# Kernel optimization log

Hardware: AMD Instinct MI355X
Metric: run time of the kernel (lower is better)

## Reference

```python
import jax, jax.numpy as jnp
import numpy as np
import math

N, E = 50000, 1600000
IN, HID, OUT, ED, H = 128, 32, 64, 64, 4
HC = H * HID  # 128, input dim of second layer


def setup_inputs() -> dict:
    key = jax.random.key(0)
    ks = jax.random.split(key, 32)
    w = lambda k, shape: (jax.random.normal(k, shape, jnp.float32) * 0.05)
    inp = {
        "x": w(ks[0], (N, IN)),
        "edge_feats": w(ks[1], (E, ED)),
        "edge_index": jax.random.randint(ks[2], (2, E), 0, N, jnp.int32),
        # layer 1: TransformerConv(IN -> HID, heads=H, concat=True, edge_dim=ED)
        "Wq1": w(ks[3], (IN, HC)), "bq1": w(ks[4], (HC,)),
        "Wk1": w(ks[5], (IN, HC)), "bk1": w(ks[6], (HC,)),
        "Wv1": w(ks[7], (IN, HC)), "bv1": w(ks[8], (HC,)),
        "We1": w(ks[9], (ED, HC)),  # lin_edge has no bias in PyG
        "Ws1": w(ks[10], (IN, HC)), "bs1": w(ks[11], (HC,)),
        # layer 2: TransformerConv(HC -> OUT, heads=1, concat=False, edge_dim=ED)
        "Wq2": w(ks[12], (HC, OUT)), "bq2": w(ks[13], (OUT,)),
        "Wk2": w(ks[14], (HC, OUT)), "bk2": w(ks[15], (OUT,)),
        "Wv2": w(ks[16], (HC, OUT)), "bv2": w(ks[17], (OUT,)),
        "We2": w(ks[18], (ED, OUT)),
        "Ws2": w(ks[19], (HC, OUT)), "bs2": w(ks[20], (OUT,)),
    }
    return inp


def tconv(x, src, dst, ef, Wq, bq, Wk, bk, Wv, bv, We, Ws, bs, heads, ch, concat):
    """PyG TransformerConv (beta=False, root_weight=True), eval mode."""
    n = x.shape[0]
    q = (x @ Wq + bq).reshape(n, heads, ch)
    k = (x @ Wk + bk).reshape(n, heads, ch)
    v = (x @ Wv + bv).reshape(n, heads, ch)
    e = (ef @ We).reshape(-1, heads, ch)           # [E,H,C]
    k_j = k[src] + e                                # gather + edge bias
    v_j = v[src] + e
    alpha = jnp.einsum("ehc,ehc->eh", q[dst], k_j) / math.sqrt(ch)  # [E,H]
    # segment softmax over destination nodes
    m = jax.lax.stop_gradient(jax.ops.segment_max(alpha, dst, num_segments=n))
    a = jnp.exp(alpha - m[dst])
    den = jax.ops.segment_sum(a, dst, num_segments=n)
    a = a / den[dst]
    msg = v_j * a[..., None]                        # [E,H,C]
    out = jax.ops.segment_sum(msg, dst, num_segments=n)  # [N,H,C]
    out = out.reshape(n, heads * ch) if concat else out.mean(axis=1)
    return out + x @ Ws + bs                        # root/skip connection


def reference(x, edge_feats, edge_index, Wq1, bq1, Wk1, bk1, Wv1, bv1, We1, Ws1, bs1,
              Wq2, bq2, Wk2, bk2, Wv2, bv2, We2, Ws2, bs2):
    src, dst = edge_index[0], edge_index[1]
    h = tconv(x, src, dst, edge_feats, Wq1, bq1, Wk1, bk1, Wv1, bv1, We1, Ws1, bs1,
              H, HID, True)
    h = jax.nn.relu(h)  # dropout=0.0 (eval) -> identity
    out = tconv(h, src, dst, edge_feats, Wq2, bq2, Wk2, bk2, Wv2, bv2, We2, Ws2, bs2,
                1, OUT, False)
    return out
```

## Files before the change

### kernel.cpp

```cpp
#include <hip/hip_runtime.h>

#define NN 50000
#define EE 1600000

__device__ inline float b2f(unsigned short u) {
    return __uint_as_float(((unsigned)u) << 16);
}
__device__ inline unsigned short f2bf(float f) {
    unsigned u = __float_as_uint(f);
    unsigned r = 0x7fffu + ((u >> 16) & 1u);
    return (unsigned short)((u + r) >> 16);
}
__device__ inline void stv(float* p, size_t i, float v) { p[i] = v; }
__device__ inline void stv(unsigned short* p, size_t i, float v) { p[i] = f2bf(v); }

__global__ void sniff_kernel(const void* w, int* flags) {
    int lane = threadIdx.x;
    const unsigned short* u = (const unsigned short*)w;
    int bad = 0;
    for (int i = lane; i < 256; i += 64) {
        float f = b2f(u[i]);
        if (!(fabsf(f) < 2.0f)) bad++;
    }
    unsigned long long m = __ballot(bad > 0);
    if (lane == 0) {
        flags[0] = (__popcll(m) > 8) ? 1 : 0;
        flags[1] = 0;
    }
}

struct WTab {
    const void* p[18];
    int off[18];
    int sz[18];
};
__global__ void __launch_bounds__(256) convert_kernel(WTab t, const int* __restrict__ flags,
                                                      unsigned short* __restrict__ dst) {
    int f32 = flags[0];
    int ti = blockIdx.y;
    int i = blockIdx.x * 256 + threadIdx.x;
    if (i < t.sz[ti]) {
        dst[t.off[ti] + i] = f32 ? f2bf(((const float*)t.p[ti])[i])
                                 : ((const unsigned short*)t.p[ti])[i];
    }
}

__global__ void __launch_bounds__(256) count_kernel(const int* __restrict__ dst,
                                                    int* __restrict__ cnt) {
    int e = blockIdx.x * 256 + threadIdx.x;
    if (e < EE) atomicAdd(&cnt[dst[e]], 1);
}

__global__ void __launch_bounds__(1024) scan_kernel(int* __restrict__ cntfill,
                                                    int* __restrict__ rowptr) {
    __shared__ int s[1024];
    __shared__ int carry_s;
    int tid = threadIdx.x;
    if (tid == 0) carry_s = 0;
    __syncthreads();
    for (int base = 0; base < NN; base += 4096) {
        int i0 = base + tid * 4;
        int v0 = (i0 + 0 < NN) ? cntfill[i0 + 0] : 0;
        int v1 = (i0 + 1 < NN) ? cntfill[i0 + 1] : 0;
        int v2 = (i0 + 2 < NN) ? cntfill[i0 + 2] : 0;
        int v3 = (i0 + 3 < NN) ? cntfill[i0 + 3] : 0;
        int tsum = v0 + v1 + v2 + v3;
        s[tid] = tsum;
        __syncthreads();
        for (int off = 1; off < 1024; off <<= 1) {
            int t = (tid >= off) ? s[tid - off] : 0;
            __syncthreads();
            s[tid] += t;
            __syncthreads();
        }
        int carry = carry_s;
        int excl = carry + s[tid] - tsum;
        int e0 = excl, e1 = excl + v0, e2 = e1 + v1, e3 = e2 + v2;
        if (i0 + 0 < NN) { rowptr[i0 + 0] = e0; cntfill[i0 + 0] = e0; }
        if (i0 + 1 < NN) { rowptr[i0 + 1] = e1; cntfill[i0 + 1] = e1; }
        if (i0 + 2 < NN) { rowptr[i0 + 2] = e2; cntfill[i0 + 2] = e2; }
        if (i0 + 3 < NN) { rowptr[i0 + 3] = e3; cntfill[i0 + 3] = e3; }
        __syncthreads();
        if (tid == 1023) carry_s = carry + s[1023];
        __syncthreads();
    }
    if (tid == 0) rowptr[NN] = carry_s;
}

__global__ void __launch_bounds__(256) fill_kernel(const int* __restrict__ dst,
                                                   int* __restrict__ cntfill,
                                                   int* __restrict__ perm) {
    int e = blockIdx.x * 256 + threadIdx.x;
    if (e < EE) {
        int p = atomicAdd(&cntfill[dst[e]], 1);
        perm[p] = e;
    }
}

template <typename TO, int K, int OD, int TR>
__global__ void __launch_bounds__(256) gemm_node(const void* __restrict__ X,
                                                 const int* __restrict__ flagp,
                                                 const unsigned short* __restrict__ W,
                                                 const unsigned short* __restrict__ bias,
                                                 TO* __restrict__ C, int nrows,
                                                 int ldc, int cstride, int coff) {
    constexpr int TRP = TR + 4;
    __shared__ unsigned short Ws[K * OD];
    __shared__ float Xs[K * TRP];
    int tid = threadIdx.x;
    int xf32 = *flagp;
    for (int i = tid; i < K * OD; i += 256) Ws[i] = W[i];
    int row0 = blockIdx.x * TR;
    const float* Xf = (const float*)X;
    const unsigned short* Xu = (const unsigned short*)X;
    for (int i = tid; i < TR * K; i += 256) {
        int r = i / K, kk = i % K;
        int rr = row0 + r;
        float vv = 0.f;
        if (rr < nrows) {
            size_t idx = (size_t)rr * K + kk;
            vv = xf32 ? Xf[idx] : b2f(Xu[idx]);
        }
        Xs[kk * TRP + r] = vv;
    }
    __syncthreads();
    constexpr int CG = OD / 4;
    int rg = tid / CG, cg = tid % CG;
    int r0 = rg * 4, c0 = cg * 4;
    float acc[4][4] = {};
#pragma unroll 4
    for (int kk = 0; kk < K; ++kk) {
        const float4 xv = *(const float4*)&Xs[kk * TRP + r0];
        ushort4 wu = *(const ushort4*)&Ws[kk * OD + c0];
        float xa[4] = {xv.x, xv.y, xv.z, xv.w};
        float wb[4] = {b2f(wu.x), b2f(wu.y), b2f(wu.z), b2f(wu.w)};
#pragma unroll
        for (int i2 = 0; i2 < 4; i2++)
#pragma unroll
            for (int j2 = 0; j2 < 4; j2++) acc[i2][j2] += xa[i2] * wb[j2];
    }
    float bb[4];
#pragma unroll
    for (int j2 = 0; j2 < 4; j2++) bb[j2] = b2f(bias[c0 + j2]);
#pragma unroll
    for (int i2 = 0; i2 < 4; i2++) {
        int rr = row0 + r0 + i2;
        if (rr < nrows) {
#pragma unroll
            for (int j2 = 0; j2 < 4; j2++)
                stv(C, (size_t)rr * ldc + (size_t)(c0 + j2) * cstride + coff,
                    acc[i2][j2] + bb[j2]);
        }
    }
}

__global__ void __launch_bounds__(256) qe1_kernel(const unsigned short* __restrict__ q,
                                                  const unsigned short* __restrict__ We,
                                                  float* __restrict__ qe) {
    __shared__ float Ws[64 * 129];
    __shared__ float qs[8 * 128];
    int tid = threadIdx.x;
    for (int i = tid; i < 64 * 128; i += 256) Ws[(i / 128) * 129 + (i % 128)] = b2f(We[i]);
    int n0 = blockIdx.x * 8;
    for (int i = tid; i < 8 * 128; i += 256) {
        int n = n0 + (i >> 7);
        qs[i] = (n < NN) ? b2f(q[(size_t)n * 128 + (i & 127)]) : 0.f;
    }
    __syncthreads();
    int h = tid >> 6, d = tid & 63;
    for (int nl = 0; nl < 8; ++nl) {
        int n = n0 + nl;
        if (n < NN) {
            float acc = 0.f;
#pragma unroll
            for (int c = 0; c < 32; ++c)
                acc += qs[nl * 128 + h * 32 + c] * Ws[d * 129 + h * 32 + c];
            qe[(size_t)n * 256 + h * 64 + d] = acc;
        }
    }
}

__global__ void __launch_bounds__(256) qe2_kernel(const unsigned short* __restrict__ q,
                                                  const unsigned short* __restrict__ We,
                                                  float* __restrict__ qe) {
    __shared__ float Ws[64 * 65];
    __shared__ float qs[4 * 64];
    int tid = threadIdx.x;
    for (int i = tid; i < 64 * 64; i += 256) Ws[(i / 64) * 65 + (i % 64)] = b2f(We[i]);
    int n0 = blockIdx.x * 4;
    {
        int n = n0 + (tid >> 6);
        qs[tid] = (n < NN) ? b2f(q[(size_t)n * 64 + (tid & 63)]) : 0.f;
    }
    __syncthreads();
    int nl = tid >> 6, d = tid & 63;
    int n = n0 + nl;
    if (n < NN) {
        float acc = 0.f;
#pragma unroll
        for (int c = 0; c < 64; ++c) acc += qs[nl * 64 + c] * Ws[d * 65 + c];
        qe[(size_t)n * 64 + d] = acc;
    }
}

__global__ void __launch_bounds__(256) node_pass1(
    const int* __restrict__ rowptr, const int* __restrict__ perm,
    const int* __restrict__ src, const unsigned short* __restrict__ q,
    const unsigned short* __restrict__ kv,
    const float* __restrict__ qe, const void* __restrict__ efp,
    const int* __restrict__ flagp, float* __restrict__ av, float* __restrict__ wef) {
    int lane = threadIdx.x & 63;
    int node = (blockIdx.x * 256 + threadIdx.x) >> 6;
    if (node >= NN) return;
    int ef32 = *flagp;
    const float* efF = (const float*)efp;
    const unsigned short* efU = (const unsigned short*)efp;
    int h = lane & 3;
    int dq = lane >> 2;
    int c1 = h * 32 + dq, c2 = c1 + 16;
    float qa = b2f(q[(size_t)node * 128 + c1]);
    float qb = b2f(q[(size_t)node * 128 + c2]);
    float4 qm = *(const float4*)(qe + (size_t)node * 256 + h * 64 + 4 * dq);
    float m = -__builtin_inff(), l = 0.f, a1 = 0.f, a2 = 0.f;
    float w0 = 0.f, w1 = 0.f, w2 = 0.f, w3 = 0.f;
    int beg = rowptr[node], end = rowptr[node + 1];
    const float rs = 0.17677669529663687f;

    int nn4 = (end - beg) & ~3;
    int lim = beg + nn4;
    int i = beg;
    int ee[4], ss[4];
    if (nn4 > 0) {
#pragma unroll
        for (int u = 0; u < 4; ++u) ee[u] = perm[i + u];
#pragma unroll
        for (int u = 0; u < 4; ++u) ss[u] = src[ee[u]];
    }
    for (; i < lim; i += 4) {
        unsigned kua[4], kub[4];
        float f0[4], f1[4], f2[4], f3[4];
#pragma unroll
        for (int u = 0; u < 4; ++u) {
            const unsigned short* kr = kv + (size_t)ss[u] * 256;
            kua[u] = *(const unsigned*)(kr + 2 * c1);
            kub[u] = *(const unsigned*)(kr + 2 * c2);
        }
        if (ef32) {
#pragma unroll
            for (int u = 0; u < 4; ++u) {
                float4 fv = *(const float4*)(efF + (size_t)ee[u] * 64 + 4 * dq);
                f0[u] = fv.x; f1[u] = fv.y; f2[u] = fv.z; f3[u] = fv.w;
            }
        } else {
#pragma unroll
            for (int u = 0; u < 4; ++u) {
                ushort4 fu = *(const ushort4*)(efU + (size_t)ee[u] * 64 + 4 * dq);
                f0[u] = b2f(fu.x); f1[u] = b2f(fu.y); f2[u] = b2f(fu.z); f3[u] = b2f(fu.w);
            }
        }
        if (i + 8 <= lim) {
#pragma unroll
            for (int u = 0; u < 4; ++u) ee[u] = perm[i + 4 + u];
#pragma unroll
            for (int u = 0; u < 4; ++u) ss[u] = src[ee[u]];
        }
        float t[4];
#pragma unroll
        for (int u = 0; u < 4; ++u) {
            float ka = b2f((unsigned short)(kua[u] & 0xffffu));
            float kb = b2f((unsigned short)(kub[u] & 0xffffu));
            float tt = qa * ka + qb * kb + qm.x * f0[u] + qm.y * f1[u] +
                       qm.z * f2[u] + qm.w * f3[u];
            tt += __shfl_xor(tt, 4);
            tt += __shfl_xor(tt, 8);
            tt += __shfl_xor(tt, 16);
            tt += __shfl_xor(tt, 32);
            t[u] = tt * rs;
        }
        float mn = fmaxf(fmaxf(fmaxf(t[0], t[1]), fmaxf(t[2], t[3])), m);
        float sc = __expf(m - mn);
        float w[4];
#pragma unroll
        for (int u = 0; u < 4; ++u) w[u] = __expf(t[u] - mn);
        m = mn;
        l = l * sc + ((w[0] + w[1]) + (w[2] + w[3]));
        float sa1 = 0.f, sa2 = 0.f, sw0 = 0.f, sw1 = 0.f, sw2 = 0.f, sw3 = 0.f;
#pragma unroll
        for (int u = 0; u < 4; ++u) {
            float va = b2f((unsigned short)(kua[u] >> 16));
            float vb = b2f((unsigned short)(kub[u] >> 16));
            sa1 += w[u] * va; sa2 += w[u] * vb;
            sw0 += w[u] * f0[u]; sw1 += w[u] * f1[u];
            sw2 += w[u] * f2[u]; sw3 += w[u] * f3[u];
        }
        a1 = a1 * sc + sa1; a2 = a2 * sc + sa2;
        w0 = w0 * sc + sw0; w1 = w1 * sc + sw1;
        w2 = w2 * sc + sw2; w3 = w3 * sc + sw3;
    }
    for (; i < end; ++i) {
        int e = perm[i];
        int sj = src[e];
        const unsigned short* kr = kv + (size_t)sj * 256;
        unsigned kua = *(const unsigned*)(kr + 2 * c1);
        unsigned kub = *(const unsigned*)(kr + 2 * c2);
        float f0s, f1s, f2s, f3s;
        if (ef32) {
            float4 fv = *(const float4*)(efF + (size_t)e * 64 + 4 * dq);
            f0s = fv.x; f1s = fv.y; f2s = fv.z; f3s = fv.w;
        } else {
            ushort4 fu = *(const ushort4*)(efU + (size_t)e * 64 + 4 * dq);
            f0s = b2f(fu.x); f1s = b2f(fu.y); f2s = b2f(fu.z); f3s = b2f(fu.w);
        }
        float ka = b2f((unsigned short)(kua & 0xffffu));
        float kb = b2f((unsigned short)(kub & 0xffffu));
        float tt = qa * ka + qb * kb + qm.x * f0s + qm.y * f1s + qm.z * f2s + qm.w * f3s;
        tt += __shfl_xor(tt, 4);
        tt += __shfl_xor(tt, 8);
        tt += __shfl_xor(tt, 16);
        tt += __shfl_xor(tt, 32);
        float alpha = tt * rs;
        float mn = fmaxf(m, alpha);
        float sc = __expf(m - mn);
        float w = __expf(alpha - mn);
        m = mn;
        l = l * sc + w;
        float va = b2f((unsigned short)(kua >> 16));
        float vb = b2f((unsigned short)(kub >> 16));
        a1 = a1 * sc + w * va;
        a2 = a2 * sc + w * vb;
        w0 = w0 * sc + w * f0s; w1 = w1 * sc + w * f1s;
        w2 = w2 * sc + w * f2s; w3 = w3 * sc + w * f3s;
    }
    float inv = (l > 0.f) ? 1.f / l : 0.f;
    av[(size_t)node * 128 + c1] = a1 * inv;
    av[(size_t)node * 128 + c2] = a2 * inv;
    float4 wout = make_float4(w0 * inv, w1 * inv, w2 * inv, w3 * inv);
    *(float4*)(wef + (size_t)node * 256 + h * 64 + 4 * dq) = wout;
}

__global__ void __launch_bounds__(256) node_pass2(
    const int* __restrict__ rowptr, const int* __restrict__ perm,
    const int* __restrict__ src, const unsigned short* __restrict__ q,
    const unsigned short* __restrict__ kv,
    const float* __restrict__ qe, const void* __restrict__ efp,
    const int* __restrict__ flagp, float* __restrict__ av, float* __restrict__ wef) {
    int lane = threadIdx.x & 63;
    int node = (blockIdx.x * 256 + threadIdx.x) >> 6;
    if (node >= NN) return;
    int ef32 = *flagp;
    const float* efF = (const float*)efp;
    const unsigned short* efU = (const unsigned short*)efp;
    float qa = b2f(q[(size_t)node * 64 + lane]);
    float qj = qe[(size_t)node * 64 + lane];
    float m = -__builtin_inff(), l = 0.f, a1 = 0.f, w0 = 0.f;
    int beg = rowptr[node], end = rowptr[node + 1];

    int nn4 = (end - beg) & ~3;
    int lim = beg + nn4;
    int i = beg;
    int ee[4], ss[4];
    if (nn4 > 0) {
#pragma unroll
        for (int u = 0; u < 4; ++u) ee[u] = perm[i + u];
#pragma unroll
        for (int u = 0; u < 4; ++u) ss[u] = src[ee[u]];
    }
    for (; i < lim; i += 4) {
        unsigned ku[4];
        float fj[4];
#pragma unroll
        for (int u = 0; u < 4; ++u)
            ku[u] = *(const unsigned*)(kv + (size_t)ss[u] * 128 + 2 * lane);
        if (ef32) {
#pragma unroll
            for (int u = 0; u < 4; ++u) fj[u] = efF[(size_t)ee[u] * 64 + lane];
        } else {
#pragma unroll
            for (int u = 0; u < 4; ++u) fj[u] = b2f(efU[(size_t)ee[u] * 64 + lane]);
        }
        if (i + 8 <= lim) {
#pragma unroll
            for (int u = 0; u < 4; ++u) ee[u] = perm[i + 4 + u];
#pragma unroll
            for (int u = 0; u < 4; ++u) ss[u] = src[ee[u]];
        }
        float t[4];
#pragma unroll
        for (int u = 0; u < 4; ++u) {
            float kk = b2f((unsigned short)(ku[u] & 0xffffu));
            float tt = qa * kk + qj * fj[u];
            tt += __shfl_xor(tt, 1);
            tt += __shfl_xor(tt, 2);
            tt += __shfl_xor(tt, 4);
            tt += __shfl_xor(tt, 8);
            tt += __shfl_xor(tt, 16);
            tt += __shfl_xor(tt, 32);
            t[u] = tt * 0.125f;
        }
        float mn = fmaxf(fmaxf(fmaxf(t[0], t[1]), fmaxf(t[2], t[3])), m);
        float sc = __expf(m - mn);
        float w[4];
#pragma unroll
        for (int u = 0; u < 4; ++u) w[u] = __expf(t[u] - mn);
        m = mn;
        l = l * sc + ((w[0] + w[1]) + (w[2] + w[3]));
        float sa = 0.f, sw = 0.f;
#pragma unroll
        for (int u = 0; u < 4; ++u) {
            float vv = b2f((unsigned short)(ku[u] >> 16));
            sa += w[u] * vv;
            sw += w[u] * fj[u];
        }
        a1 = a1 * sc + sa;
        w0 = w0 * sc + sw;
    }
    for (; i < end; ++i) {
        int e = perm[i];
        int sj = src[e];
        unsigned ku = *(const unsigned*)(kv + (size_t)sj * 128 + 2 * lane);
        float fj = ef32 ? efF[(size_t)e * 64 + lane] : b2f(efU[(size_t)e * 64 + lane]);
        float kk = b2f((unsigned short)(ku & 0xffffu));
        float tt = qa * kk + qj * fj;
        tt += __shfl_xor(tt, 1);
        tt += __shfl_xor(tt, 2);
        tt += __shfl_xor(tt, 4);
        tt += __shfl_xor(tt, 8);
        tt += __shfl_xor(tt, 16);
        tt += __shfl_xor(tt, 32);
        float alpha = tt * 0.125f;
        float mn = fmaxf(m, alpha);
        float sc = __expf(m - mn);
        float w = __expf(alpha - mn);
        m = mn;
        l = l * sc + w;
        float vv = b2f((unsigned short)(ku >> 16));
        a1 = a1 * sc + w * vv;
        w0 = w0 * sc + w * fj;
    }
    float inv = (l > 0.f) ? 1.f / l : 0.f;
    av[(size_t)node * 64 + lane] = a1 * inv;
    wef[(size_t)node * 64 + lane] = w0 * inv;
}

__global__ void __launch_bounds__(256) ep1_kernel(const float* __restrict__ av,
                                                  const float* __restrict__ wef,
                                                  const float* __restrict__ s1,
                                                  const unsigned short* __restrict__ We,
                                                  unsigned short* __restrict__ hout) {
    __shared__ float Ws[64 * 128];
    int tid = threadIdx.x;
    for (int i = tid; i < 64 * 128; i += 256) Ws[i] = b2f(We[i]);
    __syncthreads();
    int nl = tid >> 7;
    int c = tid & 127;
    int g = c >> 5;
    for (int it = 0; it < 8; ++it) {
        int n = blockIdx.x * 16 + it * 2 + nl;
        if (n < NN) {
            const float* wr = wef + (size_t)n * 256 + g * 64;
            float acc = 0.f;
#pragma unroll
            for (int d = 0; d < 64; ++d) acc += wr[d] * Ws[d * 128 + c];
            float val = av[(size_t)n * 128 + c] + acc + s1[(size_t)n * 128 + c];
            hout[(size_t)n * 128 + c] = f2bf(fmaxf(val, 0.f));
        }
    }
}

__global__ void __launch_bounds__(256) ep2_kernel(const float* __restrict__ av,
                                                  const float* __restrict__ wef,
                                                  const float* __restrict__ s2,
                                                  const unsigned short* __restrict__ We,
                                                  float* __restrict__ out) {
    __shared__ float Ws[64 * 64];
    int tid = threadIdx.x;
    for (int i = tid; i < 64 * 64; i += 256) Ws[i] = b2f(We[i]);
    __syncthreads();
    int nl = tid >> 6;
    int c = tid & 63;
    for (int it = 0; it < 4; ++it) {
        int n = blockIdx.x * 16 + it * 4 + nl;
        if (n < NN) {
            const float* wr = wef + (size_t)n * 64;
            float acc = 0.f;
#pragma unroll
            for (int d = 0; d < 64; ++d) acc += wr[d] * Ws[d * 64 + c];
            float val = av[(size_t)n * 64 + c] + acc + s2[(size_t)n * 64 + c];
            out[(size_t)n * 64 + c] = val;
        }
    }
}

extern "C" void kernel_launch(void* const* d_in, const int* in_sizes, int n_in,
                              void* d_out, int out_size, void* d_ws, size_t ws_size,
                              hipStream_t stream) {
    (void)in_sizes; (void)n_in; (void)out_size; (void)ws_size;
    const int* eidx = (const int*)d_in[2];
    const int* src = eidx;
    const int* dst = eidx + EE;

    char* p = (char*)d_ws;
    auto alloc = [&](size_t bytes) {
        void* r = (void*)p;
        p += (bytes + 255) & ~(size_t)255;
        return r;
    };
    unsigned short* wts = (unsigned short*)alloc(111360 * 2);
    int* flags          = (int*)alloc(256);
    int* rowptr         = (int*)alloc((size_t)(NN + 1) * 4);
    int* cntfill        = (int*)alloc((size_t)(NN + 1) * 4);
    int* perm           = (int*)alloc((size_t)EE * 4);
    unsigned short* q1  = (unsigned short*)alloc((size_t)NN * 128 * 2);
    unsigned short* kv1 = (unsigned short*)alloc((size_t)NN * 256 * 2);
    float* qe           = (float*)alloc((size_t)NN * 256 * 4);
    float* av           = (float*)alloc((size_t)NN * 128 * 4);
    float* wef          = (float*)alloc((size_t)NN * 256 * 4);

    WTab tab;
    int off = 0;
    const int wsz[18] = {16384, 128, 16384, 128, 16384, 128, 8192, 16384, 128,
                         8192, 64, 8192, 64, 8192, 64, 4096, 8192, 64};
    int offs[18];
    for (int i = 0; i < 18; ++i) {
        tab.p[i] = d_in[3 + i];
        tab.sz[i] = wsz[i];
        tab.off[i] = off;
        offs[i] = off;
        off += wsz[i];
    }
    const unsigned short* Wq1c = wts + offs[0];
    const unsigned short* bq1c = wts + offs[1];
    const unsigned short* Wk1c = wts + offs[2];
    const unsigned short* bk1c = wts + offs[3];
    const unsigned short* Wv1c = wts + offs[4];
    const unsigned short* bv1c = wts + offs[5];
    const unsigned short* We1c = wts + offs[6];
    const unsigned short* Ws1c = wts + offs[7];
    const unsigned short* bs1c = wts + offs[8];
    const unsigned short* Wq2c = wts + offs[9];
    const unsigned short* bq2c = wts + offs[10];
    const unsigned short* Wk2c = wts + offs[11];
    const unsigned short* bk2c = wts + offs[12];
    const unsigned short* Wv2c = wts + offs[13];
    const unsigned short* bv2c = wts + offs[14];
    const unsigned short* We2c = wts + offs[15];
    const unsigned short* Ws2c = wts + offs[16];
    const unsigned short* bs2c = wts + offs[17];

    hipMemsetAsync(cntfill, 0, (size_t)(NN + 1) * 4, stream);
    sniff_kernel<<<1, 64, 0, stream>>>(d_in[3], flags);
    convert_kernel<<<dim3(64, 18), 256, 0, stream>>>(tab, flags, wts);
    count_kernel<<<EE / 256, 256, 0, stream>>>(dst, cntfill);
    scan_kernel<<<1, 1024, 0, stream>>>(cntfill, rowptr);
    fill_kernel<<<EE / 256, 256, 0, stream>>>(dst, cntfill, perm);

    int g1 = (NN + 31) / 32;
    gemm_node<unsigned short, 128, 128, 32><<<g1, 256, 0, stream>>>(d_in[0], flags, Wq1c, bq1c, q1, NN, 128, 1, 0);
    gemm_node<unsigned short, 128, 128, 32><<<g1, 256, 0, stream>>>(d_in[0], flags, Wk1c, bk1c, kv1, NN, 256, 2, 0);
    gemm_node<unsigned short, 128, 128, 32><<<g1, 256, 0, stream>>>(d_in[0], flags, Wv1c, bv1c, kv1, NN, 256, 2, 1);
    qe1_kernel<<<(NN + 7) / 8, 256, 0, stream>>>(q1, We1c, qe);
    node_pass1<<<(NN + 3) / 4, 256, 0, stream>>>(rowptr, perm, src, q1, kv1, qe,
                                                 d_in[1], flags, av, wef);
    float* s1 = qe;
    gemm_node<float, 128, 128, 32><<<g1, 256, 0, stream>>>(d_in[0], flags, Ws1c, bs1c, s1, NN, 128, 1, 0);
    unsigned short* h = kv1;
    ep1_kernel<<<(NN + 15) / 16, 256, 0, stream>>>(av, wef, s1, We1c, h);

    unsigned short* q2 = q1;
    unsigned short* kv2 = kv1 + (size_t)NN * 128;
    float* s2 = qe;
    float* qe2 = av;
    float* av2 = av + (size_t)NN * 64;
    float* wef2 = wef;
    int g2 = (NN + 63) / 64;
    gemm_node<unsigned short, 128, 64, 64><<<g2, 256, 0, stream>>>(h, flags + 1, Wq2c, bq2c, q2, NN, 64, 1, 0);
    gemm_node<unsigned short, 128, 64, 64><<<g2, 256, 0, stream>>>(h, flags + 1, Wk2c, bk2c, kv2, NN, 128, 2, 0);
    gemm_node<unsigned short, 128, 64, 64><<<g2, 256, 0, stream>>>(h, flags + 1, Wv2c, bv2c, kv2, NN, 128, 2, 1);
    gemm_node<float, 128, 64, 64><<<g2, 256, 0, stream>>>(h, flags + 1, Ws2c, bs2c, s2, NN, 64, 1, 0);
    qe2_kernel<<<(NN + 3) / 4, 256, 0, stream>>>(q2, We2c, qe2);
    node_pass2<<<(NN + 3) / 4, 256, 0, stream>>>(rowptr, perm, src, q2, kv2, qe2,
                                                 d_in[1], flags, av2, wef2);
    ep2_kernel<<<(NN + 15) / 16, 256, 0, stream>>>(av2, wef2, s2, We2c,
                                                   (float*)d_out);
}
```

Before: 1.676 ms.

## Pre-permute edge features and sources into CSR order, double-buffer neighbor loads

Adds an edge_gather kernel that writes src indices and bf16 edge features in destination-sorted order once. Both node passes then read these contiguously instead of going through perm and gathering fp32 edge rows twice. Layer-1 K/V are stored in an interleaved layout so one 8-byte load fetches both k and v values per lane. The node loops are restructured into an A/B double-buffered prefetch pipeline. The trade-off is an extra 200MB-class permute write/read pass and bf16 rounding of edge features when they arrive as fp32.

```diff
diff --git a/kernel.cpp b/kernel.cpp
--- a/kernel.cpp
+++ b/kernel.cpp
@@ -97,7 +97,36 @@
     }
 }
 
-template <typename TO, int K, int OD, int TR>
+__global__ void __launch_bounds__(256) edge_gather(const int* __restrict__ perm,
+                                                   const int* __restrict__ src,
+                                                   const void* __restrict__ efp,
+                                                   const int* __restrict__ flagp,
+                                                   int* __restrict__ src_perm,
+                                                   unsigned short* __restrict__ efperm) {
+    int ef32 = *flagp;
+    int tid = threadIdx.x;
+    int j = tid & 15;
+    int local = tid >> 4;
+    const float* efF = (const float*)efp;
+    const unsigned short* efU = (const unsigned short*)efp;
+    for (int pass = 0; pass < 4; ++pass) {
+        int i = blockIdx.x * 64 + pass * 16 + local;
+        if (i < EE) {
+            int e = perm[i];
+            if (j == 0) src_perm[i] = src[e];
+            ushort4 o;
+            if (ef32) {
+                float4 f = *(const float4*)(efF + (size_t)e * 64 + j * 4);
+                o.x = f2bf(f.x); o.y = f2bf(f.y); o.z = f2bf(f.z); o.w = f2bf(f.w);
+            } else {
+                o = *(const ushort4*)(efU + (size_t)e * 64 + j * 4);
+            }
+            *(ushort4*)(efperm + (size_t)i * 64 + j * 4) = o;
+        }
+    }
+}
+
+template <typename TO, int K, int OD, int TR, int LAYOUT = 0>
 __global__ void __launch_bounds__(256) gemm_node(const void* __restrict__ X,
                                                  const int* __restrict__ flagp,
                                                  const unsigned short* __restrict__ W,
@@ -147,9 +176,19 @@
         int rr = row0 + r0 + i2;
         if (rr < nrows) {
 #pragma unroll
-            for (int j2 = 0; j2 < 4; j2++)
-                stv(C, (size_t)rr * ldc + (size_t)(c0 + j2) * cstride + coff,
-                    acc[i2][j2] + bb[j2]);
+            for (int j2 = 0; j2 < 4; j2++) {
+                size_t idx;
+                if constexpr (LAYOUT == 0) {
+                    idx = (size_t)rr * ldc + (size_t)(c0 + j2) * cstride + coff;
+                } else {
+                    int c = c0 + j2;
+                    int hh = c >> 5, r = c & 31;
+                    idx = (size_t)rr * 256 +
+                          (size_t)((hh * 16 + (r & 15)) * 4 + (r >> 4) +
+                                   (LAYOUT == 2 ? 2 : 0));
+                }
+                stv(C, idx, acc[i2][j2] + bb[j2]);
+            }
         }
     }
 }
@@ -203,21 +242,59 @@
     }
 }
 
+__device__ __forceinline__ void np1_step(const uint2 (&kvd)[4], const ushort4 (&efd)[4],
+                                         float qa, float qb, const float4& qm, float rs,
+                                         float& m, float& l, float& a1, float& a2,
+                                         float& w0, float& w1, float& w2, float& w3) {
+    float t[4];
+    float f0[4], f1[4], f2[4], f3[4];
+#pragma unroll
+    for (int u = 0; u < 4; ++u) {
+        float ka = b2f((unsigned short)(kvd[u].x & 0xffffu));
+        float kb = b2f((unsigned short)(kvd[u].x >> 16));
+        f0[u] = b2f(efd[u].x); f1[u] = b2f(efd[u].y);
+        f2[u] = b2f(efd[u].z); f3[u] = b2f(efd[u].w);
+        float tt = qa * ka + qb * kb + qm.x * f0[u] + qm.y * f1[u] +
+                   qm.z * f2[u] + qm.w * f3[u];
+        tt += __shfl_xor(tt, 4);
+        tt += __shfl_xor(tt, 8);
+        tt += __shfl_xor(tt, 16);
+        tt += __shfl_xor(tt, 32);
+        t[u] = tt * rs;
+    }
+    float mn = fmaxf(fmaxf(fmaxf(t[0], t[1]), fmaxf(t[2], t[3])), m);
+    float sc = __expf(m - mn);
+    float w[4];
+#pragma unroll
+    for (int u = 0; u < 4; ++u) w[u] = __expf(t[u] - mn);
+    m = mn;
+    l = l * sc + ((w[0] + w[1]) + (w[2] + w[3]));
+    float sa1 = 0.f, sa2 = 0.f, sw0 = 0.f, sw1 = 0.f, sw2 = 0.f, sw3 = 0.f;
+#pragma unroll
+    for (int u = 0; u < 4; ++u) {
+        float va = b2f((unsigned short)(kvd[u].y & 0xffffu));
+        float vb = b2f((unsigned short)(kvd[u].y >> 16));
+        sa1 += w[u] * va; sa2 += w[u] * vb;
+        sw0 += w[u] * f0[u]; sw1 += w[u] * f1[u];
+        sw2 += w[u] * f2[u]; sw3 += w[u] * f3[u];
+    }
+    a1 = a1 * sc + sa1; a2 = a2 * sc + sa2;
+    w0 = w0 * sc + sw0; w1 = w1 * sc + sw1;
+    w2 = w2 * sc + sw2; w3 = w3 * sc + sw3;
+}
+
 __global__ void __launch_bounds__(256) node_pass1(
-    const int* __restrict__ rowptr, const int* __restrict__ perm,
-    const int* __restrict__ src, const unsigned short* __restrict__ q,
-    const unsigned short* __restrict__ kv,
-    const float* __restrict__ qe, const void* __restrict__ efp,
-    const int* __restrict__ flagp, float* __restrict__ av, float* __restrict__ wef) {
+    const int* __restrict__ rowptr, const int* __restrict__ srcp,
+    const unsigned short* __restrict__ q, const unsigned short* __restrict__ kv,
+    const float* __restrict__ qe, const unsigned short* __restrict__ efperm,
+    float* __restrict__ av, float* __restrict__ wef) {
     int lane = threadIdx.x & 63;
     int node = (blockIdx.x * 256 + threadIdx.x) >> 6;
     if (node >= NN) return;
-    int ef32 = *flagp;
-    const float* efF = (const float*)efp;
-    const unsigned short* efU = (const unsigned short*)efp;
     int h = lane & 3;
     int dq = lane >> 2;
     int c1 = h * 32 + dq, c2 = c1 + 16;
+    int kvoff = (h * 16 + dq) * 4;
     float qa = b2f(q[(size_t)node * 128 + c1]);
     float qb = b2f(q[(size_t)node * 128 + c2]);
     float4 qm = *(const float4*)(qe + (size_t)node * 256 + h * 64 + 4 * dq);
@@ -225,94 +302,72 @@
     float w0 = 0.f, w1 = 0.f, w2 = 0.f, w3 = 0.f;
     int beg = rowptr[node], end = rowptr[node + 1];
     const float rs = 0.17677669529663687f;
-
-    int nn4 = (end - beg) & ~3;
-    int lim = beg + nn4;
-    int i = beg;
-    int ee[4], ss[4];
-    if (nn4 > 0) {
-#pragma unroll
-        for (int u = 0; u < 4; ++u) ee[u] = perm[i + u];
-#pragma unroll
-        for (int u = 0; u < 4; ++u) ss[u] = src[ee[u]];
-    }
-    for (; i < lim; i += 4) {
-        unsigned kua[4], kub[4];
-        float f0[4], f1[4], f2[4], f3[4];
-#pragma unroll
-        for (int u = 0; u < 4; ++u) {
-            const unsigned short* kr = kv + (size_t)ss[u] * 256;
-            kua[u] = *(const unsigned*)(kr + 2 * c1);
-            kub[u] = *(const unsigned*)(kr + 2 * c2);
-        }
-        if (ef32) {
-#pragma unroll
-            for (int u = 0; u < 4; ++u) {
-                float4 fv = *(const float4*)(efF + (size_t)ee[u] * 64 + 4 * dq);
-                f0[u] = fv.x; f1[u] = fv.y; f2[u] = fv.z; f3[u] = fv.w;
+    int ng = (end - beg) >> 2;
+
+    int ssA[4], ssB[4];
+    uint2 kvA[4], kvB[4];
+    ushort4 efA[4], efB[4];
+
+    if (ng > 0) {
+#pragma unroll
+        for (int u = 0; u < 4; ++u) ssA[u] = srcp[beg + u];
+#pragma unroll
+        for (int u = 0; u < 4; ++u)
+            kvA[u] = *(const uint2*)(kv + (size_t)ssA[u] * 256 + kvoff);
+#pragma unroll
+        for (int u = 0; u < 4; ++u)
+            efA[u] = *(const ushort4*)(efperm + (size_t)(beg + u) * 64 + 4 * dq);
+        if (ng > 1) {
+#pragma unroll
+            for (int u = 0; u < 4; ++u) ssB[u] = srcp[beg + 4 + u];
+        }
+        int g = 0;
+        while (true) {
+            bool nextB = (g + 1 < ng);
+            if (nextB) {
+                int ib = beg + ((g + 1) << 2);
+#pragma unroll
+                for (int u = 0; u < 4; ++u)
+                    kvB[u] = *(const uint2*)(kv + (size_t)ssB[u] * 256 + kvoff);
+#pragma unroll
+                for (int u = 0; u < 4; ++u)
+                    efB[u] = *(const ushort4*)(efperm + (size_t)(ib + u) * 64 + 4 * dq);
+                if (g + 2 < ng) {
+                    int ib2 = beg + ((g + 2) << 2);
+#pragma unroll
+                    for (int u = 0; u < 4; ++u) ssA[u] = srcp[ib2 + u];
+                }
             }
-        } else {
-#pragma unroll
-            for (int u = 0; u < 4; ++u) {
-                ushort4 fu = *(const ushort4*)(efU + (size_t)ee[u] * 64 + 4 * dq);
-                f0[u] = b2f(fu.x); f1[u] = b2f(fu.y); f2[u] = b2f(fu.z); f3[u] = b2f(fu.w);
+            np1_step(kvA, efA, qa, qb, qm, rs, m, l, a1, a2, w0, w1, w2, w3);
+            if (!nextB) { ++g; break; }
+            ++g;
+            bool nextA = (g + 1 < ng);
+            if (nextA) {
+                int ib = beg + ((g + 1) << 2);
+#pragma unroll
+                for (int u = 0; u < 4; ++u)
+                    kvA[u] = *(const uint2*)(kv + (size_t)ssA[u] * 256 + kvoff);
+#pragma unroll
+                for (int u = 0; u < 4; ++u)
+                    efA[u] = *(const ushort4*)(efperm + (size_t)(ib + u) * 64 + 4 * dq);
+                if (g + 2 < ng) {
+                    int ib2 = beg + ((g + 2) << 2);
+#pragma unroll
+                    for (int u = 0; u < 4; ++u) ssB[u] = srcp[ib2 + u];
+                }
             }
-        }
-        if (i + 8 <= lim) {
-#pragma unroll
-            for (int u = 0; u < 4; ++u) ee[u] = perm[i + 4 + u];
-#pragma unroll
-            for (int u = 0; u < 4; ++u) ss[u] = src[ee[u]];
-        }
-        float t[4];
-#pragma unroll
-        for (int u = 0; u < 4; ++u) {
-            float ka = b2f((unsigned short)(kua[u] & 0xffffu));
-            float kb = b2f((unsigned short)(kub[u] & 0xffffu));
-            float tt = qa * ka + qb * kb + qm.x * f0[u] + qm.y * f1[u] +
-                       qm.z * f2[u] + qm.w * f3[u];
-            tt += __shfl_xor(tt, 4);
-            tt += __shfl_xor(tt, 8);
-            tt += __shfl_xor(tt, 16);
-            tt += __shfl_xor(tt, 32);
-            t[u] = tt * rs;
-        }
-        float mn = fmaxf(fmaxf(fmaxf(t[0], t[1]), fmaxf(t[2], t[3])), m);
-        float sc = __expf(m - mn);
-        float w[4];
-#pragma unroll
-        for (int u = 0; u < 4; ++u) w[u] = __expf(t[u] - mn);
-        m = mn;
-        l = l * sc + ((w[0] + w[1]) + (w[2] + w[3]));
-        float sa1 = 0.f, sa2 = 0.f, sw0 = 0.f, sw1 = 0.f, sw2 = 0.f, sw3 = 0.f;
-#pragma unroll
-        for (int u = 0; u < 4; ++u) {
-            float va = b2f((unsigned short)(kua[u] >> 16));
-            float vb = b2f((unsigned short)(kub[u] >> 16));
-            sa1 += w[u] * va; sa2 += w[u] * vb;
-            sw0 += w[u] * f0[u]; sw1 += w[u] * f1[u];
-            sw2 += w[u] * f2[u]; sw3 += w[u] * f3[u];
-        }
-        a1 = a1 * sc + sa1; a2 = a2 * sc + sa2;
-        w0 = w0 * sc + sw0; w1 = w1 * sc + sw1;
-        w2 = w2 * sc + sw2; w3 = w3 * sc + sw3;
-    }
-    for (; i < end; ++i) {
-        int e = perm[i];
-        int sj = src[e];
-        const unsigned short* kr = kv + (size_t)sj * 256;
-        unsigned kua = *(const unsigned*)(kr + 2 * c1);
-        unsigned kub = *(const unsigned*)(kr + 2 * c2);
-        float f0s, f1s, f2s, f3s;
-        if (ef32) {
-            float4 fv = *(const float4*)(efF + (size_t)e * 64 + 4 * dq);
-            f0s = fv.x; f1s = fv.y; f2s = fv.z; f3s = fv.w;
-        } else {
-            ushort4 fu = *(const ushort4*)(efU + (size_t)e * 64 + 4 * dq);
-            f0s = b2f(fu.x); f1s = b2f(fu.y); f2s = b2f(fu.z); f3s = b2f(fu.w);
-        }
-        float ka = b2f((unsigned short)(kua & 0xffffu));
-        float kb = b2f((unsigned short)(kub & 0xffffu));
+            np1_step(kvB, efB, qa, qb, qm, rs, m, l, a1, a2, w0, w1, w2, w3);
+            if (!nextA) { ++g; break; }
+            ++g;
+        }
+    }
+    for (int i = beg + (ng << 2); i < end; ++i) {
+        int sj = srcp[i];
+        uint2 kd = *(const uint2*)(kv + (size_t)sj * 256 + kvoff);
+        ushort4 fu = *(const ushort4*)(efperm + (size_t)i * 64 + 4 * dq);
+        float f0s = b2f(fu.x), f1s = b2f(fu.y), f2s = b2f(fu.z), f3s = b2f(fu.w);
+        float ka = b2f((unsigned short)(kd.x & 0xffffu));
+        float kb = b2f((unsigned short)(kd.x >> 16));
         float tt = qa * ka + qb * kb + qm.x * f0s + qm.y * f1s + qm.z * f2s + qm.w * f3s;
         tt += __shfl_xor(tt, 4);
         tt += __shfl_xor(tt, 8);
@@ -324,8 +379,8 @@
         float w = __expf(alpha - mn);
         m = mn;
         l = l * sc + w;
-        float va = b2f((unsigned short)(kua >> 16));
-        float vb = b2f((unsigned short)(kub >> 16));
+        float va = b2f((unsigned short)(kd.y & 0xffffu));
+        float vb = b2f((unsigned short)(kd.y >> 16));
         a1 = a1 * sc + w * va;
         a2 = a2 * sc + w * vb;
         w0 = w0 * sc + w * f0s; w1 = w1 * sc + w * f1s;
@@ -338,87 +393,113 @@
     *(float4*)(wef + (size_t)node * 256 + h * 64 + 4 * dq) = wout;
 }
 
+__device__ __forceinline__ void np2_step(const unsigned (&ku)[4], const unsigned short (&fe)[4],
+                                         float qa, float qj,
+                                         float& m, float& l, float& a1, float& w0) {
+    float t[4], fj[4];
+#pragma unroll
+    for (int u = 0; u < 4; ++u) {
+        float kk = b2f((unsigned short)(ku[u] & 0xffffu));
+        fj[u] = b2f(fe[u]);
+        float tt = qa * kk + qj * fj[u];
+        tt += __shfl_xor(tt, 1);
+        tt += __shfl_xor(tt, 2);
+        tt += __shfl_xor(tt, 4);
+        tt += __shfl_xor(tt, 8);
+        tt += __shfl_xor(tt, 16);
+        tt += __shfl_xor(tt, 32);
+        t[u] = tt * 0.125f;
+    }
+    float mn = fmaxf(fmaxf(fmaxf(t[0], t[1]), fmaxf(t[2], t[3])), m);
+    float sc = __expf(m - mn);
+    float w[4];
+#pragma unroll
+    for (int u = 0; u < 4; ++u) w[u] = __expf(t[u] - mn);
+    m = mn;
+    l = l * sc + ((w[0] + w[1]) + (w[2] + w[3]));
+    float sa = 0.f, sw = 0.f;
+#pragma unroll
+    for (int u = 0; u < 4; ++u) {
+        float vv = b2f((unsigned short)(ku[u] >> 16));
+        sa += w[u] * vv;
+        sw += w[u] * fj[u];
+    }
+    a1 = a1 * sc + sa;
+    w0 = w0 * sc + sw;
+}
+
 __global__ void __launch_bounds__(256) node_pass2(
-    const int* __restrict__ rowptr, const int* __restrict__ perm,
-    const int* __restrict__ src, const unsigned short* __restrict__ q,
-    const unsigned short* __restrict__ kv,
-    const float* __restrict__ qe, const void* __restrict__ efp,
-    const int* __restrict__ flagp, float* __restrict__ av, float* __restrict__ wef) {
+    const int* __restrict__ rowptr, const int* __restrict__ srcp,
+    const unsigned short* __restrict__ q, const unsigned short* __restrict__ kv,
+    const float* __restrict__ qe, const unsigned short* __restrict__ efperm,
+    float* __restrict__ av, float* __restrict__ wef) {
     int lane = threadIdx.x & 63;
     int node = (blockIdx.x * 256 + threadIdx.x) >> 6;
     if (node >= NN) return;
-    int ef32 = *flagp;
-    const float* efF = (const float*)efp;
-    const unsigned short* efU = (const unsigned short*)efp;
     float qa = b2f(q[(size_t)node * 64 + lane]);
     float qj = qe[(size_t)node * 64 + lane];
     float m = -__builtin_inff(), l = 0.f, a1 = 0.f, w0 = 0.f;
     int beg = rowptr[node], end = rowptr[node + 1];
-
-    int nn4 = (end - beg) & ~3;
-    int lim = beg + nn4;
-    int i = beg;
-    int ee[4], ss[4];
-    if (nn4 > 0) {
-#pragma unroll
-        for (int u = 0; u < 4; ++u) ee[u] = perm[i + u];
-#pragma unroll
-        for (int u = 0; u < 4; ++u) ss[u] = src[ee[u]];
-    }
-    for (; i < lim; i += 4) {
-        unsigned ku[4];
-        float fj[4];
+    int ng = (end - beg) >> 2;
+
+    int ssA[4], ssB[4];
+    unsigned kuA[4], kuB[4];
+    unsigned short feA[4], feB[4];
+
+    if (ng > 0) {
+#pragma unroll
+        for (int u = 0; u < 4; ++u) ssA[u] = srcp[beg + u];
 #pragma unroll
         for (int u = 0; u < 4; ++u)
-            ku[u] = *(const unsigned*)(kv + (size_t)ss[u] * 128 + 2 * lane);
-        if (ef32) {
-#pragma unroll
-            for (int u = 0; u < 4; ++u) fj[u] = efF[(size_t)ee[u] * 64 + lane];
-        } else {
-#pragma unroll
-            for (int u = 0; u < 4; ++u) fj[u] = b2f(efU[(size_t)ee[u] * 64 + lane]);
-        }
-        if (i + 8 <= lim) {
-#pragma unroll
-            for (int u = 0; u < 4; ++u) ee[u] = perm[i + 4 + u];
-#pragma unroll
-            for (int u = 0; u < 4; ++u) ss[u] = src[ee[u]];
-        }
-        float t[4];
-#pragma unroll
-        for (int u = 0; u < 4; ++u) {
-            float kk = b2f((unsigned short)(ku[u] & 0xffffu));
-            float tt = qa * kk + qj * fj[u];
-            tt += __shfl_xor(tt, 1);
-            tt += __shfl_xor(tt, 2);
-            tt += __shfl_xor(tt, 4);
-            tt += __shfl_xor(tt, 8);
-            tt += __shfl_xor(tt, 16);
-            tt += __shfl_xor(tt, 32);
-            t[u] = tt * 0.125f;
-        }
-        float mn = fmaxf(fmaxf(fmaxf(t[0], t[1]), fmaxf(t[2], t[3])), m);
-        float sc = __expf(m - mn);
-        float w[4];
-#pragma unroll
-        for (int u = 0; u < 4; ++u) w[u] = __expf(t[u] - mn);
-        m = mn;
-        l = l * sc + ((w[0] + w[1]) + (w[2] + w[3]));
-        float sa = 0.f, sw = 0.f;
-#pragma unroll
-        for (int u = 0; u < 4; ++u) {
-            float vv = b2f((unsigned short)(ku[u] >> 16));
-            sa += w[u] * vv;
-            sw += w[u] * fj[u];
-        }
-        a1 = a1 * sc + sa;
-        w0 = w0 * sc + sw;
-    }
-    for (; i < end; ++i) {
-        int e = perm[i];
-        int sj = src[e];
+            kuA[u] = *(const unsigned*)(kv + (size_t)ssA[u] * 128 + 2 * lane);
+#pragma unroll
+        for (int u = 0; u < 4; ++u) feA[u] = efperm[(size_t)(beg + u) * 64 + lane];
+        if (ng > 1) {
+#pragma unroll
+            for (int u = 0; u < 4; ++u) ssB[u] = srcp[beg + 4 + u];
+        }
+        int g = 0;
+        while (true) {
+            bool nextB = (g + 1 < ng);
+            if (nextB) {
+                int ib = beg + ((g + 1) << 2);
+#pragma unroll
+                for (int u = 0; u < 4; ++u)
+                    kuB[u] = *(const unsigned*)(kv + (size_t)ssB[u] * 128 + 2 * lane);
+#pragma unroll
+                for (int u = 0; u < 4; ++u) feB[u] = efperm[(size_t)(ib + u) * 64 + lane];
+                if (g + 2 < ng) {
+                    int ib2 = beg + ((g + 2) << 2);
+#pragma unroll
+                    for (int u = 0; u < 4; ++u) ssA[u] = srcp[ib2 + u];
+                }
+            }
+            np2_step(kuA, feA, qa, qj, m, l, a1, w0);
+            if (!nextB) { ++g; break; }
+            ++g;
+            bool nextA = (g + 1 < ng);
+            if (nextA) {
+                int ib = beg + ((g + 1) << 2);
+#pragma unroll
+                for (int u = 0; u < 4; ++u)
+                    kuA[u] = *(const unsigned*)(kv + (size_t)ssA[u] * 128 + 2 * lane);
+#pragma unroll
+                for (int u = 0; u < 4; ++u) feA[u] = efperm[(size_t)(ib + u) * 64 + lane];
+                if (g + 2 < ng) {
+                    int ib2 = beg + ((g + 2) << 2);
+#pragma unroll
+                    for (int u = 0; u < 4; ++u) ssB[u] = srcp[ib2 + u];
+                }
+            }
+            np2_step(kuB, feB, qa, qj, m, l, a1, w0);
+            if (!nextA) { ++g; break; }
+            ++g;
+        }
+    }
+    for (int i = beg + (ng << 2); i < end; ++i) {
+        int sj = srcp[i];
         unsigned ku = *(const unsigned*)(kv + (size_t)sj * 128 + 2 * lane);
-        float fj = ef32 ? efF[(size_t)e * 64 + lane] : b2f(efU[(size_t)e * 64 + lane]);
+        float fj = b2f(efperm[(size_t)i * 64 + lane]);
         float kk = b2f((unsigned short)(ku & 0xffffu));
         float tt = qa * kk + qj * fj;
         tt += __shfl_xor(tt, 1);
@@ -510,6 +591,8 @@
     int* rowptr         = (int*)alloc((size_t)(NN + 1) * 4);
     int* cntfill        = (int*)alloc((size_t)(NN + 1) * 4);
     int* perm           = (int*)alloc((size_t)EE * 4);
+    int* src_perm       = (int*)alloc((size_t)EE * 4);
+    unsigned short* efperm = (unsigned short*)alloc((size_t)EE * 64 * 2);
     unsigned short* q1  = (unsigned short*)alloc((size_t)NN * 128 * 2);
     unsigned short* kv1 = (unsigned short*)alloc((size_t)NN * 256 * 2);
     float* qe           = (float*)alloc((size_t)NN * 256 * 4);
@@ -553,16 +636,18 @@
     count_kernel<<<EE / 256, 256, 0, stream>>>(dst, cntfill);
     scan_kernel<<<1, 1024, 0, stream>>>(cntfill, rowptr);
     fill_kernel<<<EE / 256, 256, 0, stream>>>(dst, cntfill, perm);
+    edge_gather<<<(EE + 63) / 64, 256, 0, stream>>>(perm, src, d_in[1], flags,
+                                                    src_perm, efperm);
 
     int g1 = (NN + 31) / 32;
-    gemm_node<unsigned short, 128, 128, 32><<<g1, 256, 0, stream>>>(d_in[0], flags, Wq1c, bq1c, q1, NN, 128, 1, 0);
-    gemm_node<unsigned short, 128, 128, 32><<<g1, 256, 0, stream>>>(d_in[0], flags, Wk1c, bk1c, kv1, NN, 256, 2, 0);
-    gemm_node<unsigned short, 128, 128, 32><<<g1, 256, 0, stream>>>(d_in[0], flags, Wv1c, bv1c, kv1, NN, 256, 2, 1);
+    gemm_node<unsigned short, 128, 128, 32, 0><<<g1, 256, 0, stream>>>(d_in[0], flags, Wq1c, bq1c, q1, NN, 128, 1, 0);
+    gemm_node<unsigned short, 128, 128, 32, 1><<<g1, 256, 0, stream>>>(d_in[0], flags, Wk1c, bk1c, kv1, NN, 0, 0, 0);
+    gemm_node<unsigned short, 128, 128, 32, 2><<<g1, 256, 0, stream>>>(d_in[0], flags, Wv1c, bv1c, kv1, NN, 0, 0, 0);
     qe1_kernel<<<(NN + 7) / 8, 256, 0, stream>>>(q1, We1c, qe);
-    node_pass1<<<(NN + 3) / 4, 256, 0, stream>>>(rowptr, perm, src, q1, kv1, qe,
-                                                 d_in[1], flags, av, wef);
+    node_pass1<<<(NN + 3) / 4, 256, 0, stream>>>(rowptr, src_perm, q1, kv1, qe,
+                                                 efperm, av, wef);
     float* s1 = qe;
-    gemm_node<float, 128, 128, 32><<<g1, 256, 0, stream>>>(d_in[0], flags, Ws1c, bs1c, s1, NN, 128, 1, 0);
+    gemm_node<float, 128, 128, 32, 0><<<g1, 256, 0, stream>>>(d_in[0], flags, Ws1c, bs1c, s1, NN, 128, 1, 0);
     unsigned short* h = kv1;
     ep1_kernel<<<(NN + 15) / 16, 256, 0, stream>>>(av, wef, s1, We1c, h);
 
@@ -573,13 +658,13 @@
     float* av2 = av + (size_t)NN * 64;
     float* wef2 = wef;
     int g2 = (NN + 63) / 64;
-    gemm_node<unsigned short, 128, 64, 64><<<g2, 256, 0, stream>>>(h, flags + 1, Wq2c, bq2c, q2, NN, 64, 1, 0);
-    gemm_node<unsigned short, 128, 64, 64><<<g2, 256, 0, stream>>>(h, flags + 1, Wk2c, bk2c, kv2, NN, 128, 2, 0);
-    gemm_node<unsigned short, 128, 64, 64><<<g2, 256, 0, stream>>>(h, flags + 1, Wv2c, bv2c, kv2, NN, 128, 2, 1);
-    gemm_node<float, 128, 64, 64><<<g2, 256, 0, stream>>>(h, flags + 1, Ws2c, bs2c, s2, NN, 64, 1, 0);
+    gemm_node<unsigned short, 128, 64, 64, 0><<<g2, 256, 0, stream>>>(h, flags + 1, Wq2c, bq2c, q2, NN, 64, 1, 0);
+    gemm_node<unsigned short, 128, 64, 64, 0><<<g2, 256, 0, stream>>>(h, flags + 1, Wk2c, bk2c, kv2, NN, 128, 2, 0);
+    gemm_node<unsigned short, 128, 64, 64, 0><<<g2, 256, 0, stream>>>(h, flags + 1, Wv2c, bv2c, kv2, NN, 128, 2, 1);
+    gemm_node<float, 128, 64, 64, 0><<<g2, 256, 0, stream>>>(h, flags + 1, Ws2c, bs2c, s2, NN, 64, 1, 0);
     qe2_kernel<<<(NN + 3) / 4, 256, 0, stream>>>(q2, We2c, qe2);
-    node_pass2<<<(NN + 3) / 4, 256, 0, stream>>>(rowptr, perm, src, q2, kv2, qe2,
-                                                 d_in[1], flags, av2, wef2);
+    node_pass2<<<(NN + 3) / 4, 256, 0, stream>>>(rowptr, src_perm, q2, kv2, qe2,
+                                                 efperm, av2, wef2);
     ep2_kernel<<<(NN + 15) / 16, 256, 0, stream>>>(av2, wef2, s2, We2c,
                                                    (float*)d_out);
 }
```

Result: slower. 1.744 ms (+4.1%).
